# Kernel tuning notes

Measured on AMD Instinct MI355X. Metric: run time of the kernel, lower is better.

Reference implementation:

```python
import jax, jax.numpy as jnp
import numpy as np

T = 4096          # prefill tokens (single sequence)
HK = 16           # key heads
HV = 32           # value heads
DK = 128          # key head dim
DV = 128          # value head dim
K = 4             # causal conv kernel width
QKV = 2 * HK * DK + HV * DV  # 8192


def setup_inputs() -> dict:
    key = jax.random.key(0)
    k1, k2, k3, k4, k5, k6 = jax.random.split(key, 6)
    return {
        "mixed_qkv": jax.random.normal(k1, (T, QKV), dtype=jnp.float32),
        "a": jax.random.normal(k2, (T, HV), dtype=jnp.float32),
        "b": jax.random.normal(k3, (T, HV), dtype=jnp.float32),
        "conv_w": jax.random.normal(k4, (QKV, K), dtype=jnp.float32) * 0.2,
        "dt_bias": jax.random.normal(k5, (HV,), dtype=jnp.float32),
        "alog": jax.random.normal(k6, (HV,), dtype=jnp.float32),
    }


def _l2norm(x, eps=1e-6):
    return x * jax.lax.rsqrt(jnp.sum(x * x, axis=-1, keepdims=True) + eps)


def _forward(mixed_qkv, a, b, conv_w, dt_bias, alog):
    # --- causal depthwise conv1d (zero initial conv state) + SiLU ---
    xp = jnp.pad(mixed_qkv, ((K - 1, 0), (0, 0)))  # [T+K-1, QKV]
    y = sum(conv_w[None, :, j] * xp[j:j + T] for j in range(K))  # [T, QKV]
    x = jax.nn.silu(y)

    # --- split q/k/v ---
    q, k_, v = jnp.split(x, [HK * DK, 2 * HK * DK], axis=-1)
    q = q.reshape(T, HK, DK)
    k_ = k_.reshape(T, HK, DK)
    v = v.reshape(T, HV, DV)

    # use_qk_l2norm_in_kernel=True: L2-norm q,k; scale q by dk^-0.5
    q = _l2norm(q) * (DK ** -0.5)
    k_ = _l2norm(k_)

    # GQA: repeat key-head q/k to value-head count
    grp = HV // HK
    q = jnp.repeat(q, grp, axis=1)   # [T, HV, DK]
    k_ = jnp.repeat(k_, grp, axis=1)  # [T, HV, DK]

    # --- fused_gdn_gating ---
    g = -jnp.exp(alog)[None, :] * jax.nn.softplus(a + dt_bias[None, :])  # [T, HV]
    beta = jax.nn.sigmoid(b)                                             # [T, HV]

    # --- gated delta-rule recurrence (equiv. to chunk_gated_delta_rule) ---
    S0 = jnp.zeros((HV, DK, DV), dtype=mixed_qkv.dtype)

    def step(S, inp):
        qt, kt, vt, gt, bt = inp
        S = S * jnp.exp(gt)[:, None, None]                 # gated decay
        pred = jnp.einsum('hk,hkv->hv', kt, S)             # k^T S
        delta = (vt - pred) * bt[:, None]                  # beta-scaled error
        S = S + jnp.einsum('hk,hv->hkv', kt, delta)        # delta update
        o = jnp.einsum('hk,hkv->hv', qt, S)                # query readout
        return S, o

    _, out = jax.lax.scan(step, S0, (q, k_, v, g, beta))
    return out  # [T, HV, DV]


def reference(mixed_qkv, a, b, conv_w, dt_bias, alog):
    return _forward(mixed_qkv, a, b, conv_w, dt_bias, alog)
```

## Files before the change

kernel.cpp:

```cpp
#include <hip/hip_runtime.h>

#define T_LEN 4096
#define HKn   16
#define HVn   32
#define DKn   128
#define DVn   128
#define QKVn  8192
#define NCH   64
#define CS    64

typedef __attribute__((ext_vector_type(8))) short short8;
typedef __attribute__((ext_vector_type(4))) float f32x4;
typedef __attribute__((ext_vector_type(4))) unsigned u32x4;

#define OFF_QSH  ((size_t)0)
#define OFF_QSL  ((size_t)16777216)
#define OFF_KSH  ((size_t)33554432)
#define OFF_KSL  ((size_t)50331648)
#define OFF_KTH  ((size_t)67108864)
#define OFF_KTL  ((size_t)83886080)
#define OFF_VA   ((size_t)100663296)
#define OFF_GBL  ((size_t)167772160)
#define OFF_G    ((size_t)168820736)
#define OFF_WH   ((size_t)169345024)
#define OFF_WL   ((size_t)202899456)
#define OFF_MH   ((size_t)236453888)
#define OFF_ML   ((size_t)253231104)

template <int CTRL>
__device__ __forceinline__ float dpp_add(float x) {
    int v = __builtin_amdgcn_update_dpp(0, __float_as_int(x), CTRL, 0xF, 0xF, true);
    return x + __int_as_float(v);
}
__device__ __forceinline__ float reduce32g(float x) {
    x = dpp_add<0x128>(x); x = dpp_add<0x124>(x);
    x = dpp_add<0x122>(x); x = dpp_add<0x121>(x);
    int v = __builtin_amdgcn_ds_swizzle(__float_as_int(x), 0x401F);
    return x + __int_as_float(v);
}
__device__ __forceinline__ unsigned short bf16rne(float f) {
    unsigned x = __float_as_uint(f);
    return (unsigned short)((x + 0x7FFFu + ((x >> 16) & 1u)) >> 16);
}
__device__ __forceinline__ float bf16tof(unsigned short h) {
    return __uint_as_float(((unsigned)h) << 16);
}
__device__ __forceinline__ void bsplit(float f, unsigned short& h, unsigned short& l) {
    h = bf16rne(f);
    l = bf16rne(f - bf16tof(h));
}
__device__ __forceinline__ unsigned packsplit(float f) {
    unsigned short h, l; bsplit(f, h, l);
    return ((unsigned)h << 16) | (unsigned)l;
}
__device__ __forceinline__ f32x4 MF(short8 a, short8 b, f32x4 c) {
    return __builtin_amdgcn_mfma_f32_16x16x32_bf16(a, b, c, 0, 0, 0);
}
__device__ __forceinline__ void unpack8(u32x4 x0, u32x4 x1, short8& hi, short8& lo) {
    union { u32x4 u; short8 s; } H, L;
    H.u[0] = __builtin_amdgcn_perm(x0.y, x0.x, 0x07060302u);
    L.u[0] = __builtin_amdgcn_perm(x0.y, x0.x, 0x05040100u);
    H.u[1] = __builtin_amdgcn_perm(x0.w, x0.z, 0x07060302u);
    L.u[1] = __builtin_amdgcn_perm(x0.w, x0.z, 0x05040100u);
    H.u[2] = __builtin_amdgcn_perm(x1.y, x1.x, 0x07060302u);
    L.u[2] = __builtin_amdgcn_perm(x1.y, x1.x, 0x05040100u);
    H.u[3] = __builtin_amdgcn_perm(x1.w, x1.z, 0x07060302u);
    L.u[3] = __builtin_amdgcn_perm(x1.w, x1.z, 0x05040100u);
    hi = H.s; lo = L.s;
}
#define SB0() __builtin_amdgcn_sched_barrier(0)
#define BARL() do { \
    asm volatile("s_waitcnt lgkmcnt(0)" ::: "memory"); \
    __builtin_amdgcn_s_barrier(); \
    asm volatile("" ::: "memory"); \
} while (0)
#define WAITV0() do { \
    asm volatile("s_waitcnt vmcnt(0)" ::: "memory"); \
    SB0(); \
} while (0)
#define WAITL0() do { \
    asm volatile("s_waitcnt lgkmcnt(0)" ::: "memory"); \
    SB0(); \
} while (0)

typedef __attribute__((address_space(3))) void lds_t;
typedef const __attribute__((address_space(1))) void gbl_t;
__device__ __forceinline__ void load_lds16(const void* g, void* l) {
    __builtin_amdgcn_global_load_lds((gbl_t*)g, (lds_t*)l, 16, 0, 0);
}
__device__ __forceinline__ void load_lds4(const void* g, void* l) {
    __builtin_amdgcn_global_load_lds((gbl_t*)g, (lds_t*)l, 4, 0, 0);
}

__global__ __launch_bounds__(256) void k_gate(
    const float* __restrict__ a, const float* __restrict__ b,
    const float* __restrict__ dt_bias, const float* __restrict__ alog,
    float2* __restrict__ gbl)
{
    const int i = blockIdx.x * 256 + threadIdx.x;
    if (i < T_LEN * HVn) {
        const int h = i >> 12, t = i & (T_LEN - 1);
        const float av = a[(size_t)t * HVn + h];
        const float bv = b[(size_t)t * HVn + h];
        const float xv = av + dt_bias[h];
        const float sp = fmaxf(xv, 0.f) + log1pf(expf(-fabsf(xv)));
        const float g  = -expf(alog[h]) * sp;
        const float beta = 1.f / (1.f + expf(-bv));
        gbl[(size_t)h * T_LEN + t] = make_float2(beta, g);
    }
}

__global__ __launch_bounds__(128) void k_conv(
    const float* __restrict__ x, const float* __restrict__ w,
    const float* __restrict__ bgate,
    unsigned short* __restrict__ qsh, unsigned short* __restrict__ qsl,
    unsigned short* __restrict__ ksh, unsigned short* __restrict__ ksl,
    float* __restrict__ va2)
{
    const int t = blockIdx.x, seg = blockIdx.y, d = threadIdx.x;
    const int c = seg * 128 + d;
    const float4 w4 = ((const float4*)w)[c];
    float acc;
    if (t >= 3) {
        const float* xc = x + (size_t)(t - 3) * QKVn + c;
        acc = fmaf(w4.x, xc[0], fmaf(w4.y, xc[(size_t)QKVn],
              fmaf(w4.z, xc[(size_t)2 * QKVn], w4.w * xc[(size_t)3 * QKVn])));
    } else {
        float a0 = (t - 3 >= 0) ? x[(size_t)(t - 3) * QKVn + c] : 0.f;
        float a1 = (t - 2 >= 0) ? x[(size_t)(t - 2) * QKVn + c] : 0.f;
        float a2 = (t - 1 >= 0) ? x[(size_t)(t - 1) * QKVn + c] : 0.f;
        float a3 = x[(size_t)t * QKVn + c];
        acc = fmaf(w4.x, a0, fmaf(w4.y, a1, fmaf(w4.z, a2, w4.w * a3)));
    }
    const float y = acc / (1.f + expf(-acc));

    if (seg < 32) {
        float ss = reduce32g(y * y);
        __shared__ float part[4];
        if ((threadIdx.x & 31) == 0) part[threadIdx.x >> 5] = ss;
        __syncthreads();
        const float total = part[0] + part[1] + part[2] + part[3];
        const float r = rsqrtf(total + 1e-6f);
        float o = y * r;
        unsigned short hh, ll;
        if (seg < 16) {
            o *= 0.08838834764831845f;
            bsplit(o, hh, ll);
            const size_t idx = ((size_t)seg * T_LEN + t) * DKn + d;
            qsh[idx] = hh; qsl[idx] = ll;
        } else {
            bsplit(o, hh, ll);
            const size_t idx = ((size_t)(seg - 16) * T_LEN + t) * DKn + d;
            ksh[idx] = hh; ksl[idx] = ll;
        }
    } else {
        const int h = seg - 32;
        const float bv = bgate[(size_t)t * HVn + h];
        const float beta = 1.f / (1.f + expf(-bv));
        va2[((size_t)h * T_LEN + t) * DVn + d] = y * beta;
    }
}

__global__ __launch_bounds__(256) void k_tr(
    const unsigned short* __restrict__ ksh, const unsigned short* __restrict__ ksl,
    unsigned short* __restrict__ kth, unsigned short* __restrict__ ktl)
{
    __shared__ unsigned pk[64][65];
    const int b = blockIdx.x;
    const int kh = b >> 7, tt = (b >> 1) & 63, hh = b & 1;
    const int t0 = tt * 64, d0 = hh * 64;
    const int tid = threadIdx.x;
    #pragma unroll
    for (int e = 0; e < 16; ++e) {
        const int lin = e * 256 + tid;
        const int tl = lin >> 6, dl = lin & 63;
        const size_t o = ((size_t)kh * T_LEN + t0 + tl) * DKn + d0 + dl;
        pk[tl][dl] = ((unsigned)ksh[o] << 16) | (unsigned)ksl[o];
    }
    __syncthreads();
    #pragma unroll
    for (int e = 0; e < 16; ++e) {
        const int lin = e * 256 + tid;
        const int dl = lin >> 6, tl = lin & 63;
        const unsigned v = pk[tl][dl];
        const size_t o = ((size_t)kh * DKn + d0 + dl) * T_LEN + t0 + tl;
        kth[o] = (unsigned short)(v >> 16);
        ktl[o] = (unsigned short)(v & 0xFFFF);
    }
}

__global__ __launch_bounds__(256) void k_p1(
    const float2* __restrict__ gbl,
    const unsigned short* __restrict__ qsh, const unsigned short* __restrict__ qsl,
    const unsigned short* __restrict__ ksh, const unsigned short* __restrict__ ksl,
    float* __restrict__ va2, float* __restrict__ Gbuf,
    unsigned short* __restrict__ Wh, unsigned short* __restrict__ Wl,
    unsigned short* __restrict__ Mh, unsigned short* __restrict__ Ml)
{
    __shared__ float sA[64][68];
    __shared__ float sG[64];
    __shared__ float sB[64];
    const int blk = blockIdx.x;
    const int h = blk >> 6, ch = blk & 63;
    const int kh = h >> 1, t0 = ch * 64;
    const int tid = threadIdx.x, lane = tid & 63, wid = tid >> 6;
    const int l15 = lane & 15, lg = lane >> 4;

    if (tid < 64) {
        float2 g2 = gbl[(size_t)h * T_LEN + t0 + tid];
        sB[tid] = g2.x;
        float G = g2.y;
        #pragma unroll
        for (int s = 1; s < 64; s <<= 1) {
            float y = __int_as_float(__builtin_amdgcn_ds_bpermute((tid - s) << 2, __float_as_int(G)));
            G += (tid >= s) ? y : 0.f;
        }
        sG[tid] = G;
        Gbuf[(size_t)h * T_LEN + t0 + tid] = G;
    }
    __syncthreads();

    const char TIa[10] = {0,1,1,2,2,2,3,3,3,3};
    const char TJa[10] = {0,0,1,0,1,2,0,1,2,3};
    const size_t kbase = ((size_t)kh * T_LEN + t0) * DKn;
    for (int idx = wid; idx < 10; idx += 4) {
        const int mi = TIa[idx], nj = TJa[idx];
        f32x4 aKK = {0.f,0.f,0.f,0.f}, aQK = {0.f,0.f,0.f,0.f};
        #pragma unroll
        for (int kk = 0; kk < 4; ++kk) {
            const size_t offA = kbase + (size_t)(16*mi + l15) * DKn + 32*kk + 8*lg;
            const size_t offB = kbase + (size_t)(16*nj + l15) * DKn + 32*kk + 8*lg;
            short8 kAh = *(const short8*)(ksh + offA);
            short8 kAl = *(const short8*)(ksl + offA);
            short8 kBh = *(const short8*)(ksh + offB);
            short8 kBl = *(const short8*)(ksl + offB);
            short8 qAh = *(const short8*)(qsh + offA);
            short8 qAl = *(const short8*)(qsl + offA);
            aKK = MF(kAh,kBh,aKK); aKK = MF(kAh,kBl,aKK); aKK = MF(kAl,kBh,aKK);
            aQK = MF(qAh,kBh,aQK); aQK = MF(qAh,kBl,aQK); aQK = MF(qAl,kBh,aQK);
        }
        #pragma unroll
        for (int r = 0; r < 4; ++r) {
            const int i = 16*mi + 4*lg + r;
            const int j = 16*nj + l15;
            const float e = __expf(fminf(sG[i] - sG[j], 0.f));
            sA[i][j] = (j < i) ? sB[i] * e * aKK[r] : 0.f;
            const float mv = (j <= i) ? e * aQK[r] : 0.f;
            unsigned short mh, ml; bsplit(mv, mh, ml);
            const size_t moff = (((size_t)h * NCH + ch) * CS + i) * CS + j;
            Mh[moff] = mh; Ml[moff] = ml;
        }
    }
    __syncthreads();

    const int c = tid;
    float X[64];
    if (c < 128) {
        #pragma unroll
        for (int i = 0; i < 64; ++i)
            X[i] = va2[((size_t)h * T_LEN + t0 + i) * DVn + c];
    } else {
        const int dk = c - 128;
        #pragma unroll
        for (int i = 0; i < 64; ++i) {
            const size_t o = ((size_t)kh * T_LEN + t0 + i) * DKn + dk;
            const float kf = bf16tof(ksh[o]) + bf16tof(ksl[o]);
            X[i] = sB[i] * __expf(sG[i]) * kf;
        }
    }
    #pragma unroll
    for (int i = 1; i < 64; ++i) {
        float acc = X[i];
        const int nq = (i + 3) >> 2;
        #pragma unroll
        for (int q = 0; q < nq; ++q) {
            const f32x4 aa = *(const f32x4*)&sA[i][4*q];
            acc = fmaf(-aa[0], X[4*q+0], acc);
            acc = fmaf(-aa[1], X[4*q+1], acc);
            acc = fmaf(-aa[2], X[4*q+2], acc);
            acc = fmaf(-aa[3], X[4*q+3], acc);
        }
        X[i] = acc;
    }
    if (c < 128) {
        #pragma unroll
        for (int i = 0; i < 64; ++i)
            va2[((size_t)h * T_LEN + t0 + i) * DVn + c] = X[i];
    } else {
        const int dk = c - 128;
        #pragma unroll
        for (int i = 0; i < 64; ++i) {
            unsigned short wh, wl; bsplit(-X[i], wh, wl);
            const size_t o = (((size_t)h * NCH + ch) * CS + i) * DKn + dk;
            Wh[o] = wh; Wl[o] = wl;
        }
    }
}

#define SLOT  1024
#define OFF_GROW 28672
#define OFF_U    28928
#define WSTG  29952

__global__ __launch_bounds__(256, 1) void k_p2(
    const unsigned short* __restrict__ qsh, const unsigned short* __restrict__ qsl,
    const unsigned short* __restrict__ kth, const unsigned short* __restrict__ ktl,
    const unsigned short* __restrict__ Wh, const unsigned short* __restrict__ Wl,
    const unsigned short* __restrict__ Mh, const unsigned short* __restrict__ Ml,
    const float* __restrict__ va2, const float* __restrict__ Gbuf,
    float* __restrict__ out)
{
    __shared__ __align__(16) char stg[4][WSTG];
    __shared__ unsigned sSp[16][132];
    __shared__ unsigned sDLp[16][68];
    __shared__ unsigned sDSp[16][68];

    const int p = blockIdx.x;
    const int slot = p >> 3;
    const int h  = (p & 7) * 4 + (slot & 3);
    const int nb = slot >> 2;
    const int kh = h >> 1, n0 = nb * 16;
    const int tid = threadIdx.x, lane = tid & 63, wid = tid >> 6;
    const int l15 = lane & 15, lg = lane >> 4;

    char* wb = &stg[wid][0];

    short8 Sbh[4], Sbl[4];
    f32x4 Sc[2];
    const short8 z8 = {0,0,0,0,0,0,0,0};
    #pragma unroll
    for (int kk = 0; kk < 4; ++kk) { Sbh[kk] = z8; Sbl[kk] = z8; }
    Sc[0] = (f32x4){0.f,0.f,0.f,0.f};
    Sc[1] = (f32x4){0.f,0.f,0.f,0.f};

    auto stage_ch = [&](int ch) {
        const int t0 = ch * CS;
        const size_t wbase = (((size_t)h * NCH + ch) * CS + 16*wid + l15) * DKn + 8*lg;
        #pragma unroll
        for (int kk = 0; kk < 4; ++kk) {
            load_lds16(Wh + wbase + 32*kk, wb + (0 + kk) * SLOT);
            load_lds16(Wl + wbase + 32*kk, wb + (4 + kk) * SLOT);
        }
        const size_t kb0 = ((size_t)kh * DKn + 16*wid + l15) * T_LEN + t0 + 8*lg;
        const size_t kb1 = ((size_t)kh * DKn + 16*(wid + 4) + l15) * T_LEN + t0 + 8*lg;
        #pragma unroll
        for (int k2 = 0; k2 < 2; ++k2) {
            load_lds16(kth + kb0 + 32*k2, wb + (8  + k2) * SLOT);
            load_lds16(kth + kb1 + 32*k2, wb + (10 + k2) * SLOT);
            load_lds16(ktl + kb0 + 32*k2, wb + (12 + k2) * SLOT);
            load_lds16(ktl + kb1 + 32*k2, wb + (14 + k2) * SLOT);
        }
        const size_t qbase = ((size_t)kh * T_LEN + t0 + 16*wid + l15) * DKn + 8*lg;
        #pragma unroll
        for (int kk = 0; kk < 4; ++kk) {
            load_lds16(qsh + qbase + 32*kk, wb + (16 + kk) * SLOT);
            load_lds16(qsl + qbase + 32*kk, wb + (20 + kk) * SLOT);
        }
        const size_t mbase = (((size_t)h * NCH + ch) * CS + 16*wid + l15) * CS + 8*lg;
        #pragma unroll
        for (int k2 = 0; k2 < 2; ++k2) {
            load_lds16(Mh + mbase + 32*k2, wb + (24 + k2) * SLOT);
            load_lds16(Ml + mbase + 32*k2, wb + (26 + k2) * SLOT);
        }
        load_lds4(Gbuf + (size_t)h * T_LEN + t0 + lane, wb + OFF_GROW);
        #pragma unroll
        for (int r = 0; r < 4; ++r)
            load_lds4(va2 + ((size_t)h * T_LEN + t0 + 16*wid + 4*lg + r) * DVn + n0 + l15,
                      wb + OFF_U + r * 256);
    };

    stage_ch(0);

    #pragma unroll 1
    for (int ch = 0; ch < NCH; ++ch) {
        const int t0 = ch * CS;
        WAITV0();

        const float* gw = (const float*)(wb + OFF_GROW);
        float gr[4];
        #pragma unroll
        for (int r = 0; r < 4; ++r) gr[r] = gw[16*wid + 4*lg + r];
        const float g63 = gw[63];
        const float lam = __expf(g63);
        float scE[4], eg[4];
        #pragma unroll
        for (int r = 0; r < 4; ++r) { scE[r] = __expf(g63 - gr[r]); eg[r] = __expf(gr[r]); }
        float uf[4];
        #pragma unroll
        for (int r = 0; r < 4; ++r) uf[r] = *(const float*)(wb + OFF_U + r * 256 + lane * 4);

        f32x4 dl = {uf[0], uf[1], uf[2], uf[3]};
        #pragma unroll
        for (int kk = 0; kk < 4; ++kk) {
            const short8 wh8 = *(const short8*)(wb + (0 + kk) * SLOT + lane * 16);
            const short8 wl8 = *(const short8*)(wb + (4 + kk) * SLOT + lane * 16);
            dl = MF(wh8, Sbh[kk], dl); dl = MF(wh8, Sbl[kk], dl); dl = MF(wl8, Sbh[kk], dl);
        }

        const int cc0 = 16*wid + 4*lg;
        u32x4 pdl, pds;
        #pragma unroll
        for (int r = 0; r < 4; ++r) {
            pdl[r] = packsplit(dl[r]);
            pds[r] = packsplit(dl[r] * scE[r]);
        }
        *(u32x4*)&sDLp[l15][cc0] = pdl;
        *(u32x4*)&sDSp[l15][cc0] = pds;
        BARL();

        short8 dlh[2], dll[2], dsh[2], dsl[2];
        #pragma unroll
        for (int k2 = 0; k2 < 2; ++k2) {
            u32x4 x0 = *(const u32x4*)&sDLp[l15][32*k2 + 8*lg];
            u32x4 x1 = *(const u32x4*)&sDLp[l15][32*k2 + 8*lg + 4];
            unpack8(x0, x1, dlh[k2], dll[k2]);
            u32x4 y0 = *(const u32x4*)&sDSp[l15][32*k2 + 8*lg];
            u32x4 y1 = *(const u32x4*)&sDSp[l15][32*k2 + 8*lg + 4];
            unpack8(y0, y1, dsh[k2], dsl[k2]);
        }

        f32x4 aq = {0.f,0.f,0.f,0.f}, am = {0.f,0.f,0.f,0.f};
        #pragma unroll
        for (int kk = 0; kk < 4; ++kk) {
            const short8 qh8 = *(const short8*)(wb + (16 + kk) * SLOT + lane * 16);
            const short8 ql8 = *(const short8*)(wb + (20 + kk) * SLOT + lane * 16);
            aq = MF(qh8, Sbh[kk], aq); aq = MF(qh8, Sbl[kk], aq); aq = MF(ql8, Sbh[kk], aq);
        }
        #pragma unroll
        for (int k2 = 0; k2 < 2; ++k2) {
            const short8 mh8 = *(const short8*)(wb + (24 + k2) * SLOT + lane * 16);
            const short8 ml8 = *(const short8*)(wb + (26 + k2) * SLOT + lane * 16);
            am = MF(mh8, dlh[k2], am); am = MF(mh8, dll[k2], am); am = MF(ml8, dlh[k2], am);
        }
        #pragma unroll
        for (int r = 0; r < 4; ++r) {
            const int cc = cc0 + r;
            out[((size_t)(t0 + cc) * HVn + h) * DVn + n0 + l15] = fmaf(eg[r], aq[r], am[r]);
        }

        #pragma unroll
        for (int m2 = 0; m2 < 2; ++m2) {
            f32x4 t4 = {0.f,0.f,0.f,0.f};
            #pragma unroll
            for (int k2 = 0; k2 < 2; ++k2) {
                const short8 th8 = *(const short8*)(wb + (8 + 2*m2 + k2) * SLOT + lane * 16);
                const short8 tl8 = *(const short8*)(wb + (12 + 2*m2 + k2) * SLOT + lane * 16);
                t4 = MF(th8, dsh[k2], t4); t4 = MF(th8, dsl[k2], t4); t4 = MF(tl8, dsh[k2], t4);
            }
            u32x4 ps;
            #pragma unroll
            for (int r = 0; r < 4; ++r) {
                Sc[m2][r] = fmaf(lam, Sc[m2][r], t4[r]);
                ps[r] = packsplit(Sc[m2][r]);
            }
            *(u32x4*)&sSp[l15][16*wid + 64*m2 + 4*lg] = ps;
        }
        BARL();

        #pragma unroll
        for (int kk = 0; kk < 4; ++kk) {
            u32x4 z0 = *(const u32x4*)&sSp[l15][32*kk + 8*lg];
            u32x4 z1 = *(const u32x4*)&sSp[l15][32*kk + 8*lg + 4];
            unpack8(z0, z1, Sbh[kk], Sbl[kk]);
        }

        if (ch + 1 < NCH) {
            WAITL0();
            stage_ch(ch + 1);
        }
    }
}

extern "C" void kernel_launch(void* const* d_in, const int* in_sizes, int n_in,
                              void* d_out, int out_size, void* d_ws, size_t ws_size,
                              hipStream_t stream) {
    const float* mixed_qkv = (const float*)d_in[0];
    const float* a         = (const float*)d_in[1];
    const float* b         = (const float*)d_in[2];
    const float* conv_w    = (const float*)d_in[3];
    const float* dt_bias   = (const float*)d_in[4];
    const float* alog      = (const float*)d_in[5];
    float* out = (float*)d_out;
    char* ws = (char*)d_ws;

    unsigned short* qsh = (unsigned short*)(ws + OFF_QSH);
    unsigned short* qsl = (unsigned short*)(ws + OFF_QSL);
    unsigned short* ksh = (unsigned short*)(ws + OFF_KSH);
    unsigned short* ksl = (unsigned short*)(ws + OFF_KSL);
    unsigned short* kth = (unsigned short*)(ws + OFF_KTH);
    unsigned short* ktl = (unsigned short*)(ws + OFF_KTL);
    float*  va2 = (float*)(ws + OFF_VA);
    float2* gbl = (float2*)(ws + OFF_GBL);
    float*  Gbf = (float*)(ws + OFF_G);
    unsigned short* Wh = (unsigned short*)(ws + OFF_WH);
    unsigned short* Wl = (unsigned short*)(ws + OFF_WL);
    unsigned short* Mh = (unsigned short*)(ws + OFF_MH);
    unsigned short* Ml = (unsigned short*)(ws + OFF_ML);

    k_gate<<<(T_LEN * HVn + 255) / 256, 256, 0, stream>>>(a, b, dt_bias, alog, gbl);

    dim3 cgrid(T_LEN, 64);
    k_conv<<<cgrid, 128, 0, stream>>>(mixed_qkv, conv_w, b, qsh, qsl, ksh, ksl, va2);

    k_tr<<<2048, 256, 0, stream>>>(ksh, ksl, kth, ktl);

    k_p1<<<HVn * NCH, 256, 0, stream>>>(gbl, qsh, qsl, ksh, ksl, va2, Gbf, Wh, Wl, Mh, Ml);

    k_p2<<<HVn * 8, 256, 0, stream>>>(qsh, qsl, kth, ktl, Wh, Wl, Mh, Ml, va2, Gbf, out);
}
```

Baseline: 581.2 us.

## Vectorize conv kernel and split MFMA chains, reorder state update before readout

The conv kernel now has each thread handle four channels with 128-bit loads and stores, so each block covers four heads and the grid shrinks fourfold. In the recurrent kernel, the three split-precision MFMA products accumulate into independent registers and are summed at the end, which shortens the dependency chains. The state update is moved ahead of the output readout so the next chunk's staging can be issued earlier and overlap the readout. Splitting the accumulators changes the floating-point summation order, and each wave's L2 norm relies on a 32-lane reduction covering exactly one head.

```diff
diff --git a/kernel.cpp b/kernel.cpp
--- a/kernel.cpp
+++ b/kernel.cpp
@@ -12,6 +12,7 @@
 typedef __attribute__((ext_vector_type(8))) short short8;
 typedef __attribute__((ext_vector_type(4))) float f32x4;
 typedef __attribute__((ext_vector_type(4))) unsigned u32x4;
+typedef __attribute__((ext_vector_type(4))) unsigned short us4;
 
 #define OFF_QSH  ((size_t)0)
 #define OFF_QSL  ((size_t)16777216)
@@ -117,47 +118,70 @@
     unsigned short* __restrict__ ksh, unsigned short* __restrict__ ksl,
     float* __restrict__ va2)
 {
-    const int t = blockIdx.x, seg = blockIdx.y, d = threadIdx.x;
-    const int c = seg * 128 + d;
-    const float4 w4 = ((const float4*)w)[c];
-    float acc;
+    const int t = blockIdx.x, seg = blockIdx.y, tid = threadIdx.x;
+    const int c0 = seg * 512 + tid * 4;
+
+    f32x4 wv[4];
+    #pragma unroll
+    for (int j = 0; j < 4; ++j) wv[j] = *(const f32x4*)(w + (size_t)(c0 + j) * 4);
+
+    f32x4 acc;
     if (t >= 3) {
-        const float* xc = x + (size_t)(t - 3) * QKVn + c;
-        acc = fmaf(w4.x, xc[0], fmaf(w4.y, xc[(size_t)QKVn],
-              fmaf(w4.z, xc[(size_t)2 * QKVn], w4.w * xc[(size_t)3 * QKVn])));
+        const float* xb = x + (size_t)(t - 3) * QKVn + c0;
+        const f32x4 x0 = *(const f32x4*)(xb);
+        const f32x4 x1 = *(const f32x4*)(xb + QKVn);
+        const f32x4 x2 = *(const f32x4*)(xb + 2 * QKVn);
+        const f32x4 x3 = *(const f32x4*)(xb + 3 * QKVn);
+        #pragma unroll
+        for (int j = 0; j < 4; ++j)
+            acc[j] = fmaf(wv[j][0], x0[j], fmaf(wv[j][1], x1[j],
+                     fmaf(wv[j][2], x2[j], wv[j][3] * x3[j])));
     } else {
-        float a0 = (t - 3 >= 0) ? x[(size_t)(t - 3) * QKVn + c] : 0.f;
-        float a1 = (t - 2 >= 0) ? x[(size_t)(t - 2) * QKVn + c] : 0.f;
-        float a2 = (t - 1 >= 0) ? x[(size_t)(t - 1) * QKVn + c] : 0.f;
-        float a3 = x[(size_t)t * QKVn + c];
-        acc = fmaf(w4.x, a0, fmaf(w4.y, a1, fmaf(w4.z, a2, w4.w * a3)));
-    }
-    const float y = acc / (1.f + expf(-acc));
-
-    if (seg < 32) {
-        float ss = reduce32g(y * y);
-        __shared__ float part[4];
-        if ((threadIdx.x & 31) == 0) part[threadIdx.x >> 5] = ss;
-        __syncthreads();
-        const float total = part[0] + part[1] + part[2] + part[3];
-        const float r = rsqrtf(total + 1e-6f);
-        float o = y * r;
-        unsigned short hh, ll;
-        if (seg < 16) {
-            o *= 0.08838834764831845f;
-            bsplit(o, hh, ll);
-            const size_t idx = ((size_t)seg * T_LEN + t) * DKn + d;
-            qsh[idx] = hh; qsl[idx] = ll;
+        f32x4 xs[4];
+        #pragma unroll
+        for (int p = 0; p < 4; ++p) {
+            const int tt = t - 3 + p;
+            if (tt >= 0) xs[p] = *(const f32x4*)(x + (size_t)tt * QKVn + c0);
+            else         xs[p] = (f32x4){0.f, 0.f, 0.f, 0.f};
+        }
+        #pragma unroll
+        for (int j = 0; j < 4; ++j)
+            acc[j] = fmaf(wv[j][0], xs[0][j], fmaf(wv[j][1], xs[1][j],
+                     fmaf(wv[j][2], xs[2][j], wv[j][3] * xs[3][j])));
+    }
+    f32x4 y;
+    #pragma unroll
+    for (int j = 0; j < 4; ++j) y[j] = acc[j] / (1.f + expf(-acc[j]));
+
+    if (seg < 8) {
+        float ss = y[0]*y[0] + y[1]*y[1] + y[2]*y[2] + y[3]*y[3];
+        ss = reduce32g(ss);
+        float r = rsqrtf(ss + 1e-6f);
+        if (seg < 4) r *= 0.08838834764831845f;
+        us4 hi, lo;
+        #pragma unroll
+        for (int j = 0; j < 4; ++j) {
+            unsigned short hh, ll; bsplit(y[j] * r, hh, ll);
+            hi[j] = hh; lo[j] = ll;
+        }
+        const int d = c0 & 127;
+        if (seg < 4) {
+            const int head = c0 >> 7;
+            const size_t idx = ((size_t)head * T_LEN + t) * DKn + d;
+            *(us4*)(qsh + idx) = hi; *(us4*)(qsl + idx) = lo;
         } else {
-            bsplit(o, hh, ll);
-            const size_t idx = ((size_t)(seg - 16) * T_LEN + t) * DKn + d;
-            ksh[idx] = hh; ksl[idx] = ll;
+            const int head = (c0 - 2048) >> 7;
+            const size_t idx = ((size_t)head * T_LEN + t) * DKn + d;
+            *(us4*)(ksh + idx) = hi; *(us4*)(ksl + idx) = lo;
         }
     } else {
-        const int h = seg - 32;
+        const int h = (c0 - 4096) >> 7;
         const float bv = bgate[(size_t)t * HVn + h];
         const float beta = 1.f / (1.f + expf(-bv));
-        va2[((size_t)h * T_LEN + t) * DVn + d] = y * beta;
+        f32x4 o;
+        #pragma unroll
+        for (int j = 0; j < 4; ++j) o[j] = y[j] * beta;
+        *(f32x4*)(va2 + ((size_t)h * T_LEN + t) * DVn + (c0 & 127)) = o;
     }
 }
 
@@ -389,13 +413,19 @@
         #pragma unroll
         for (int r = 0; r < 4; ++r) uf[r] = *(const float*)(wb + OFF_U + r * 256 + lane * 4);
 
-        f32x4 dl = {uf[0], uf[1], uf[2], uf[3]};
+        f32x4 d0 = {uf[0], uf[1], uf[2], uf[3]};
+        f32x4 d1 = {0.f,0.f,0.f,0.f}, d2 = {0.f,0.f,0.f,0.f};
         #pragma unroll
         for (int kk = 0; kk < 4; ++kk) {
             const short8 wh8 = *(const short8*)(wb + (0 + kk) * SLOT + lane * 16);
             const short8 wl8 = *(const short8*)(wb + (4 + kk) * SLOT + lane * 16);
-            dl = MF(wh8, Sbh[kk], dl); dl = MF(wh8, Sbl[kk], dl); dl = MF(wl8, Sbh[kk], dl);
-        }
+            d0 = MF(wh8, Sbh[kk], d0);
+            d1 = MF(wh8, Sbl[kk], d1);
+            d2 = MF(wl8, Sbh[kk], d2);
+        }
+        f32x4 dl;
+        #pragma unroll
+        for (int r = 0; r < 4; ++r) dl[r] = d0[r] + d1[r] + d2[r];
 
         const int cc0 = 16*wid + 4*lg;
         u32x4 pdl, pds;
@@ -419,6 +449,27 @@
             unpack8(y0, y1, dsh[k2], dsl[k2]);
         }
 
+        #pragma unroll
+        for (int m2 = 0; m2 < 2; ++m2) {
+            f32x4 t0a = {0.f,0.f,0.f,0.f}, t1a = {0.f,0.f,0.f,0.f}, t2a = {0.f,0.f,0.f,0.f};
+            #pragma unroll
+            for (int k2 = 0; k2 < 2; ++k2) {
+                const short8 th8 = *(const short8*)(wb + (8 + 2*m2 + k2) * SLOT + lane * 16);
+                const short8 tl8 = *(const short8*)(wb + (12 + 2*m2 + k2) * SLOT + lane * 16);
+                t0a = MF(th8, dsh[k2], t0a);
+                t1a = MF(th8, dsl[k2], t1a);
+                t2a = MF(tl8, dsh[k2], t2a);
+            }
+            u32x4 ps;
+            #pragma unroll
+            for (int r = 0; r < 4; ++r) {
+                Sc[m2][r] = fmaf(lam, Sc[m2][r], t0a[r] + t1a[r] + t2a[r]);
+                ps[r] = packsplit(Sc[m2][r]);
+            }
+            *(u32x4*)&sSp[l15][16*wid + 64*m2 + 4*lg] = ps;
+        }
+        BARL();
+
         f32x4 aq = {0.f,0.f,0.f,0.f}, am = {0.f,0.f,0.f,0.f};
         #pragma unroll
         for (int kk = 0; kk < 4; ++kk) {
@@ -438,35 +489,16 @@
             out[((size_t)(t0 + cc) * HVn + h) * DVn + n0 + l15] = fmaf(eg[r], aq[r], am[r]);
         }
 
-        #pragma unroll
-        for (int m2 = 0; m2 < 2; ++m2) {
-            f32x4 t4 = {0.f,0.f,0.f,0.f};
-            #pragma unroll
-            for (int k2 = 0; k2 < 2; ++k2) {
-                const short8 th8 = *(const short8*)(wb + (8 + 2*m2 + k2) * SLOT + lane * 16);
-                const short8 tl8 = *(const short8*)(wb + (12 + 2*m2 + k2) * SLOT + lane * 16);
-                t4 = MF(th8, dsh[k2], t4); t4 = MF(th8, dsl[k2], t4); t4 = MF(tl8, dsh[k2], t4);
-            }
-            u32x4 ps;
-            #pragma unroll
-            for (int r = 0; r < 4; ++r) {
-                Sc[m2][r] = fmaf(lam, Sc[m2][r], t4[r]);
-                ps[r] = packsplit(Sc[m2][r]);
-            }
-            *(u32x4*)&sSp[l15][16*wid + 64*m2 + 4*lg] = ps;
-        }
-        BARL();
+        if (ch + 1 < NCH) {
+            WAITL0();
+            stage_ch(ch + 1);
+        }
 
         #pragma unroll
         for (int kk = 0; kk < 4; ++kk) {
             u32x4 z0 = *(const u32x4*)&sSp[l15][32*kk + 8*lg];
             u32x4 z1 = *(const u32x4*)&sSp[l15][32*kk + 8*lg + 4];
             unpack8(z0, z1, Sbh[kk], Sbl[kk]);
-        }
-
-        if (ch + 1 < NCH) {
-            WAITL0();
-            stage_ch(ch + 1);
         }
     }
 }
@@ -499,7 +531,7 @@
 
     k_gate<<<(T_LEN * HVn + 255) / 256, 256, 0, stream>>>(a, b, dt_bias, alog, gbl);
 
-    dim3 cgrid(T_LEN, 64);
+    dim3 cgrid(T_LEN, 16);
     k_conv<<<cgrid, 128, 0, stream>>>(mixed_qkv, conv_w, b, qsh, qsl, ksh, ksl, va2);
 
     k_tr<<<2048, 256, 0, stream>>>(ksh, ksl, kth, ktl);
```

Result: faster. 556.2 us (-4.3%).
